# Kernel tuning notes

Measured on AMD Instinct MI355X. Metric: run time of the kernel, lower is better.

Reference implementation:

```python
import jax, jax.numpy as jnp
import numpy as np
import math

B, T, C, H = 4, 2048, 1024, 16

def setup_inputs() -> dict:
    key = jax.random.key(0)
    k1, k2, k3 = jax.random.split(key, 3)
    scale = 1.0 / math.sqrt(C)
    return {
        "x": jax.random.normal(k1, (B, T, C), dtype=jnp.float32),
        "w_attn": jax.random.normal(k2, (C, 3 * C), dtype=jnp.float32) * scale,
        "b_attn": jnp.zeros((3 * C,), dtype=jnp.float32),
        "w_proj": jax.random.normal(k3, (C, C), dtype=jnp.float32) * scale,
        "b_proj": jnp.zeros((C,), dtype=jnp.float32),
    }

def reference(x, w_attn, b_attn, w_proj, b_proj):
    Bq, Tq, Cq = x.shape
    hd = Cq // H  # head dim
    qkv = x @ w_attn + b_attn                       # [B,T,3C]
    q, k, v = jnp.split(qkv, 3, axis=-1)
    # [B,T,C] -> [B,H,T,hd]
    q = q.reshape(Bq, Tq, H, hd).transpose(0, 2, 1, 3)
    k = k.reshape(Bq, Tq, H, hd).transpose(0, 2, 1, 3)
    v = v.reshape(Bq, Tq, H, hd).transpose(0, 2, 1, 3)
    att = jnp.einsum('bhqd,bhkd->bhqk', q, k) * (1.0 / math.sqrt(hd))
    causal = jnp.tril(jnp.ones((Tq, Tq), dtype=bool))
    att = jnp.where(causal[None, None], att, -jnp.inf)
    att = jax.nn.softmax(att, axis=-1)              # dropout p=0 (eval)
    y = jnp.einsum('bhqk,bhkd->bhqd', att, v)       # [B,H,T,hd]
    y = y.transpose(0, 2, 1, 3).reshape(Bq, Tq, Cq)
    return y @ w_proj + b_proj
```

## Files before the change

### kernel.cpp

```cpp
#include <hip/hip_runtime.h>


#define T_SEQ 2048
#define NB 4
#define NH 16
#define CDIM 1024
#define HD 64
#define BH (NB * NH)
#define QSCALE 0.1803368801111204f

typedef float f32x4 __attribute__((ext_vector_type(4)));
typedef float f32x16 __attribute__((ext_vector_type(16)));
typedef __bf16 bf16x8 __attribute__((ext_vector_type(8)));
typedef unsigned short u16x8 __attribute__((ext_vector_type(8)));
typedef unsigned short u16x4 __attribute__((ext_vector_type(4)));

__device__ __forceinline__ unsigned short f2b(float f) {
    union { float f; unsigned u; } v; v.f = f;
    unsigned u = v.u;
    u += 0x7FFFu + ((u >> 16) & 1u);
    return (unsigned short)(u >> 16);
}

__device__ __forceinline__ f32x4 fzero4() {
    f32x4 z; z[0] = 0.f; z[1] = 0.f; z[2] = 0.f; z[3] = 0.f; return z;
}

__device__ __forceinline__ f32x4 mfma16(bf16x8 a, bf16x8 b, f32x4 c) {
    return __builtin_amdgcn_mfma_f32_16x16x32_bf16(a, b, c, 0, 0, 0);
}

__device__ __forceinline__ f32x16 mfma32(bf16x8 a, bf16x8 b, f32x16 c) {
    return __builtin_amdgcn_mfma_f32_32x32x16_bf16(a, b, c, 0, 0, 0);
}

__device__ __forceinline__ void gld16(const void* gp, void* lp) {
    __builtin_amdgcn_global_load_lds(
        (const __attribute__((address_space(1))) unsigned int*)gp,
        (__attribute__((address_space(3))) unsigned int*)lp, 16, 0, 0);
}

#define FENCE asm volatile("" ::: "memory")

__device__ __forceinline__ void transpose_tile(
        const float* __restrict__ in, unsigned short* __restrict__ out,
        int R, int C, int bx, int by) {
    __shared__ unsigned short tile[32][33];
    int tx = threadIdx.x & 31, ty = threadIdx.x >> 5;
    int c0 = bx * 32, r0 = by * 32;
#pragma unroll
    for (int rr = ty; rr < 32; rr += 8)
        tile[rr][tx] = f2b(in[(size_t)(r0 + rr) * C + c0 + tx]);
    __syncthreads();
#pragma unroll
    for (int rr = ty; rr < 32; rr += 8)
        out[(size_t)(c0 + rr) * R + r0 + tx] = tile[tx][rr];
}

__global__ __launch_bounds__(256) void prep_kernel(
        const float* __restrict__ x, const float* __restrict__ wa,
        const float* __restrict__ wp, unsigned short* __restrict__ xb,
        unsigned short* __restrict__ wTa, unsigned short* __restrict__ wTp) {
    int b = blockIdx.x;
    if (b < 1024) {
        int n8 = (NB * T_SEQ * CDIM) / 8;
        for (int i = b * 256 + threadIdx.x; i < n8; i += 1024 * 256) {
            const float4* p = reinterpret_cast<const float4*>(x) + (size_t)i * 2;
            float4 a = p[0], c = p[1];
            u16x8 o;
            o[0] = f2b(a.x); o[1] = f2b(a.y); o[2] = f2b(a.z); o[3] = f2b(a.w);
            o[4] = f2b(c.x); o[5] = f2b(c.y); o[6] = f2b(c.z); o[7] = f2b(c.w);
            *(reinterpret_cast<u16x8*>(xb) + i) = o;
        }
    } else if (b < 1024 + 3072) {
        int t = b - 1024;
        transpose_tile(wa, wTa, 1024, 3072, t % 96, t / 96);
    } else {
        int t = b - 4096;
        transpose_tile(wp, wTp, 1024, 1024, t % 32, t / 32);
    }
}

__global__ __launch_bounds__(256) void gemm_qkv_kernel(
        const unsigned short* __restrict__ A, const unsigned short* __restrict__ Bt,
        const float* __restrict__ bias,
        unsigned short* __restrict__ q_out, unsigned short* __restrict__ k_out,
        unsigned short* __restrict__ v_out, int M, int N, int K) {
    __shared__ alignas(16) unsigned short As[128 * 32];
    __shared__ alignas(16) unsigned short Bs[2][128 * 32];

    int tid = threadIdx.x;
    int wid = tid >> 6, lane = tid & 63;
    int g = lane >> 4, lc = lane & 15;
    int wr = (wid >> 1) * 64, wc = (wid & 1) * 64;
    int m0 = blockIdx.y * 128, n0 = blockIdx.x * 128;

    f32x4 acc[4][4];
#pragma unroll
    for (int m = 0; m < 4; ++m)
#pragma unroll
        for (int n = 0; n < 4; ++n) acc[m][n] = fzero4();

    int srow = tid >> 2;
    int scol = ((tid & 3) ^ ((srow >> 1) & 3)) * 8;
    const unsigned short* Ap = A + (size_t)(m0 + srow) * K + scol;
    const unsigned short* Bp = Bt + (size_t)(n0 + srow) * K + scol;
    int ldst = (wid * 16) * 32;
    int ldst2 = (64 + wid * 16) * 32;

#define STAGE_A(KOFF) {                                    \
        gld16(Ap + (KOFF), &As[ldst]);                     \
        gld16(Ap + (size_t)64 * K + (KOFF), &As[ldst2]); }
#define STAGE_B(BUF, KOFF) {                                       \
        gld16(Bp + (KOFF), &Bs[BUF][ldst]);                        \
        gld16(Bp + (size_t)64 * K + (KOFF), &Bs[BUF][ldst2]); }

    STAGE_B(0, 0)
    STAGE_A(0)
    STAGE_B(1, 32)

    int swz8 = (g ^ ((lc >> 1) & 3)) * 8;

    int nk = K >> 5;
    for (int it = 0; it < nk; ++it) {
        if (it + 1 < nk) { asm volatile("s_waitcnt vmcnt(2)" ::: "memory"); }
        else             { asm volatile("s_waitcnt vmcnt(0)" ::: "memory"); }
        FENCE; __builtin_amdgcn_s_barrier(); FENCE;

        bf16x8 af[4], bfr[4];
        const unsigned short* Bb = Bs[it & 1];
#pragma unroll
        for (int m = 0; m < 4; ++m)
            af[m] = *(const bf16x8*)&As[(wr + m * 16 + lc) * 32 + swz8];
#pragma unroll
        for (int n = 0; n < 4; ++n)
            bfr[n] = *(const bf16x8*)&Bb[(wc + n * 16 + lc) * 32 + swz8];

        __builtin_amdgcn_s_setprio(1);
#pragma unroll
        for (int m = 0; m < 4; ++m)
#pragma unroll
            for (int n = 0; n < 4; ++n)
                acc[m][n] = mfma16(af[m], bfr[n], acc[m][n]);
        __builtin_amdgcn_s_setprio(0);

        asm volatile("s_waitcnt lgkmcnt(0)" ::: "memory");
        FENCE; __builtin_amdgcn_s_barrier(); FENCE;
        if (it + 1 < nk) STAGE_A((it + 1) << 5)
        if (it + 2 < nk) STAGE_B(it & 1, (it + 2) << 5)
    }
#undef STAGE_A
#undef STAGE_B

#pragma unroll
    for (int m = 0; m < 4; ++m) {
        int rowb = m0 + wr + m * 16 + g * 4;
#pragma unroll
        for (int n = 0; n < 4; ++n) {
            int col = n0 + wc + n * 16 + lc;
            float bv = bias[col];
            int which = col >> 10;
            int c = col & 1023;
            int h = c >> 6, d = c & 63;
            int bh_ = (rowb >> 11) * NH + h;
            int tl = rowb & 2047;
            if (which == 2) {
                u16x4 vq;
#pragma unroll
                for (int i = 0; i < 4; ++i) vq[i] = f2b(acc[m][n][i] + bv);
                *(u16x4*)&v_out[(size_t)bh_ * (HD * T_SEQ) + (size_t)d * T_SEQ + tl] = vq;
            } else {
                unsigned short* dst = which ? k_out : q_out;
                float sc = which ? 1.0f : QSCALE;
#pragma unroll
                for (int i = 0; i < 4; ++i)
                    dst[((size_t)bh_ * T_SEQ + tl + i) * HD + d] =
                        f2b((acc[m][n][i] + bv) * sc);
            }
        }
    }
}

__global__ __launch_bounds__(256) void gemm_proj_kernel(
        const unsigned short* __restrict__ A, const unsigned short* __restrict__ Bt,
        const float* __restrict__ bias, float* __restrict__ outF, int M, int N, int K) {
    __shared__ alignas(16) unsigned short As[2][128 * 32];
    __shared__ alignas(16) unsigned short Bs[2][128 * 32];

    int tid = threadIdx.x;
    int wid = tid >> 6, lane = tid & 63;
    int g = lane >> 4, lc = lane & 15;
    int wr = (wid >> 1) * 64, wc = (wid & 1) * 64;
    int m0 = blockIdx.y * 128, n0 = blockIdx.x * 128;

    f32x4 acc[4][4];
#pragma unroll
    for (int m = 0; m < 4; ++m)
#pragma unroll
        for (int n = 0; n < 4; ++n) acc[m][n] = fzero4();

    int srow = tid >> 2;
    int scol = ((tid & 3) ^ ((srow >> 1) & 3)) * 8;
    const unsigned short* Ap = A + (size_t)(m0 + srow) * K + scol;
    const unsigned short* Bp = Bt + (size_t)(n0 + srow) * K + scol;
    int ldst = (wid * 16) * 32;
    int ldst2 = (64 + wid * 16) * 32;

#define GSTAGE(BUF, KOFF)                                      \
    gld16(Ap + (KOFF), &As[BUF][ldst]);                        \
    gld16(Ap + (size_t)64 * K + (KOFF), &As[BUF][ldst2]);      \
    gld16(Bp + (KOFF), &Bs[BUF][ldst]);                        \
    gld16(Bp + (size_t)64 * K + (KOFF), &Bs[BUF][ldst2]);

    GSTAGE(0, 0)
    GSTAGE(1, 32)

    int swz8 = (g ^ ((lc >> 1) & 3)) * 8;

    int nk = K >> 5;
    for (int it = 0; it < nk; ++it) {
        int cur = it & 1;
        if (it + 1 < nk) { asm volatile("s_waitcnt vmcnt(4)" ::: "memory"); }
        else             { asm volatile("s_waitcnt vmcnt(0)" ::: "memory"); }
        FENCE; __builtin_amdgcn_s_barrier(); FENCE;

        bf16x8 af[4], bfr[4];
#pragma unroll
        for (int m = 0; m < 4; ++m)
            af[m] = *(const bf16x8*)&As[cur][(wr + m * 16 + lc) * 32 + swz8];
#pragma unroll
        for (int n = 0; n < 4; ++n)
            bfr[n] = *(const bf16x8*)&Bs[cur][(wc + n * 16 + lc) * 32 + swz8];

        __builtin_amdgcn_s_setprio(1);
#pragma unroll
        for (int m = 0; m < 4; ++m)
#pragma unroll
            for (int n = 0; n < 4; ++n)
                acc[m][n] = mfma16(af[m], bfr[n], acc[m][n]);
        __builtin_amdgcn_s_setprio(0);

        FENCE; __builtin_amdgcn_s_barrier(); FENCE;
        if (it + 2 < nk) { GSTAGE(cur, (it + 2) << 5) }
    }
#undef GSTAGE

#pragma unroll
    for (int m = 0; m < 4; ++m) {
        int rowb = m0 + wr + m * 16 + g * 4;
#pragma unroll
        for (int n = 0; n < 4; ++n) {
            int col = n0 + wc + n * 16 + lc;
            float bv = bias[col];
#pragma unroll
            for (int i = 0; i < 4; ++i)
                outF[(size_t)(rowb + i) * N + col] = acc[m][n][i] + bv;
        }
    }
}

__global__ __launch_bounds__(512, 4) void attn32_kernel(
        const unsigned short* __restrict__ Qb, const unsigned short* __restrict__ Kb,
        const unsigned short* __restrict__ Vt, unsigned short* __restrict__ Yb) {
    __shared__ alignas(16) char smem[32768];

    int tid = threadIdx.x;
    int wid = tid >> 6, lane = tid & 63;
    int ql = lane & 31, hi = lane >> 5;
    int ql7 = ql & 7;

    int id = blockIdx.x;
    int x = id & 7;
    int k = id >> 3;
    int g = k & 7;
    if (k & 32) g = 7 - g;
    int bh = x * 8 + (k >> 3);
    size_t hb = (size_t)bh * (T_SEQ * HD);

    int qt = g * 8 + wid;
    int q0 = qt * 32;
    int ktMax = qt >> 1;
    int ntB = 4 * g + 4;

    bf16x8 qf[4];
    const unsigned short* Qp = Qb + hb + (size_t)(q0 + ql) * HD + hi * 8;
#pragma unroll
    for (int d = 0; d < 4; ++d) qf[d] = *(const bf16x8*)(Qp + d * 16);

    f32x16 zz;
#pragma unroll
    for (int rr = 0; rr < 16; ++rr) zz[rr] = 0.f;
    f32x16 o0 = zz, o1 = zz;
    float mi = -__builtin_inff(), li = 0.f;

    int r8 = lane >> 3;
    int sslot8 = ((lane & 7) ^ r8) * 8;
    const unsigned short* Kg = Kb + hb + (size_t)(wid * 8 + r8) * HD + sslot8;
    const unsigned short* Vg = Vt + hb + (size_t)(wid * 8 + r8) * T_SEQ + sslot8;

    gld16(Kg, smem + wid * 1024);
    gld16(Vg, smem + 8192 + wid * 1024);
    __syncthreads();

#define KF(K0, D) (*(const bf16x8*)&KB_[(((K0)*32 + ql) << 6) + ((((D)*2 + hi) ^ ql7) << 3)])
#define VF(DB, T) (*(const bf16x8*)&VB_[(((DB)*32 + ql) << 6) + ((((T)*2 + hi) ^ ql7) << 3)])

    for (int kt = 0; kt < ntB; ++kt) {
        int cur = kt & 1;
        bool pf = (kt + 1 < ntB);
        if (pf) {
            char* nb = smem + (cur ^ 1) * 16384;
            gld16(Kg + (size_t)(kt + 1) * 64 * HD, nb + wid * 1024);
            gld16(Vg + (kt + 1) * 64, nb + 8192 + wid * 1024);
        }
        if (pf) { asm volatile("s_waitcnt vmcnt(2)" ::: "memory"); }
        else    { asm volatile("s_waitcnt vmcnt(0)" ::: "memory"); }
        FENCE; __builtin_amdgcn_s_barrier(); FENCE;

        if (kt <= ktMax) {
            const unsigned short* KB_ = (const unsigned short*)(smem + cur * 16384);
            const unsigned short* VB_ = (const unsigned short*)(smem + cur * 16384 + 8192);
            int k0 = kt * 64;

            f32x16 s0_, s1_;
            __builtin_amdgcn_s_setprio(1);
            s0_ = mfma32(KF(0, 0), qf[0], zz);
            s0_ = mfma32(KF(0, 1), qf[1], s0_);
            s0_ = mfma32(KF(0, 2), qf[2], s0_);
            s0_ = mfma32(KF(0, 3), qf[3], s0_);
            s1_ = mfma32(KF(1, 0), qf[0], zz);
            s1_ = mfma32(KF(1, 1), qf[1], s1_);
            s1_ = mfma32(KF(1, 2), qf[2], s1_);
            s1_ = mfma32(KF(1, 3), qf[3], s1_);
            __builtin_amdgcn_s_setprio(0);

            if (kt == ktMax) {
                int qg_ = q0 + ql;
#pragma unroll
                for (int rr = 0; rr < 16; ++rr) {
                    int kof_ = k0 + 8 * (rr >> 2) + (rr & 3) + 4 * hi;
                    if (kof_ > qg_) s0_[rr] = -__builtin_inff();
                    if (kof_ + 32 > qg_) s1_[rr] = -__builtin_inff();
                }
            }

            float t_[8];
#pragma unroll
            for (int rr = 0; rr < 8; ++rr)
                t_[rr] = fmaxf(fmaxf(s0_[rr], s0_[rr + 8]), fmaxf(s1_[rr], s1_[rr + 8]));
#pragma unroll
            for (int rr = 0; rr < 4; ++rr) t_[rr] = fmaxf(t_[rr], t_[rr + 4]);
            float pm_ = fmaxf(fmaxf(t_[0], t_[1]), fmaxf(t_[2], t_[3]));
            pm_ = fmaxf(pm_, __shfl_xor(pm_, 32));

            float mn_ = mi;
            if (!__all((int)(pm_ <= mi + 8.f))) {
                mn_ = fmaxf(mi, pm_);
                float f_ = __builtin_amdgcn_exp2f(mi - mn_);
                mi = mn_;
                li *= f_;
                o0 *= f_;
                o1 *= f_;
            }
#pragma unroll
            for (int rr = 0; rr < 16; ++rr) {
                s0_[rr] = __builtin_amdgcn_exp2f(s0_[rr] - mn_);
                s1_[rr] = __builtin_amdgcn_exp2f(s1_[rr] - mn_);
            }
            float u_[8];
#pragma unroll
            for (int rr = 0; rr < 8; ++rr)
                u_[rr] = (s0_[rr] + s0_[rr + 8]) + (s1_[rr] + s1_[rr + 8]);
#pragma unroll
            for (int rr = 0; rr < 4; ++rr) u_[rr] += u_[rr + 4];
            float ps_ = (u_[0] + u_[1]) + (u_[2] + u_[3]);
            ps_ += __shfl_xor(ps_, 32);
            li += ps_;

#pragma unroll
            for (int K0_ = 0; K0_ < 2; ++K0_) {
#pragma unroll
                for (int h2_ = 0; h2_ < 2; ++h2_) {
                    float e0_ = K0_ ? s1_[8 * h2_ + 0] : s0_[8 * h2_ + 0];
                    float e1_ = K0_ ? s1_[8 * h2_ + 1] : s0_[8 * h2_ + 1];
                    float e2_ = K0_ ? s1_[8 * h2_ + 2] : s0_[8 * h2_ + 2];
                    float e3_ = K0_ ? s1_[8 * h2_ + 3] : s0_[8 * h2_ + 3];
                    float e4_ = K0_ ? s1_[8 * h2_ + 4] : s0_[8 * h2_ + 4];
                    float e5_ = K0_ ? s1_[8 * h2_ + 5] : s0_[8 * h2_ + 5];
                    float e6_ = K0_ ? s1_[8 * h2_ + 6] : s0_[8 * h2_ + 6];
                    float e7_ = K0_ ? s1_[8 * h2_ + 7] : s0_[8 * h2_ + 7];
                    unsigned a_, b_, c_, d_;
                    asm("v_cvt_pk_bf16_f32 %0, %1, %2" : "=v"(a_) : "v"(e0_), "v"(e1_));
                    asm("v_cvt_pk_bf16_f32 %0, %1, %2" : "=v"(b_) : "v"(e2_), "v"(e3_));
                    asm("v_cvt_pk_bf16_f32 %0, %1, %2" : "=v"(c_) : "v"(e4_), "v"(e5_));
                    asm("v_cvt_pk_bf16_f32 %0, %1, %2" : "=v"(d_) : "v"(e6_), "v"(e7_));
                    asm("v_permlane32_swap_b32 %0, %1" : "+v"(a_), "+v"(c_));
                    asm("v_permlane32_swap_b32 %0, %1" : "+v"(b_), "+v"(d_));
                    union { unsigned u[4]; bf16x8 v; } pf_;
                    pf_.u[0] = a_; pf_.u[1] = b_; pf_.u[2] = c_; pf_.u[3] = d_;
                    __builtin_amdgcn_s_setprio(1);
                    o0 = mfma32(VF(0, K0_ * 2 + h2_), pf_.v, o0);
                    o1 = mfma32(VF(1, K0_ * 2 + h2_), pf_.v, o1);
                    __builtin_amdgcn_s_setprio(0);
                }
            }
        }
        asm volatile("s_waitcnt lgkmcnt(0)" ::: "memory");
        FENCE; __builtin_amdgcn_s_barrier(); FENCE;
    }
#undef KF
#undef VF

    int bb = bh >> 4, h = bh & 15;
    float iv = 1.0f / li;
#pragma unroll
    for (int dblk = 0; dblk < 2; ++dblk) {
#pragma unroll
        for (int a = 0; a < 4; ++a) {
            u16x4 wv;
#pragma unroll
            for (int i = 0; i < 4; ++i)
                wv[i] = f2b((dblk ? o1[4 * a + i] : o0[4 * a + i]) * iv);
            int dq = dblk * 32 + 8 * a + 4 * hi;
            *(u16x4*)&Yb[((size_t)(bb * T_SEQ + q0 + ql)) * CDIM + h * HD + dq] = wv;
        }
    }
}

extern "C" void kernel_launch(void* const* d_in, const int* in_sizes, int n_in,
                              void* d_out, int out_size, void* d_ws, size_t ws_size,
                              hipStream_t stream) {
    const float* x      = (const float*)d_in[0];
    const float* w_attn = (const float*)d_in[1];
    const float* b_attn = (const float*)d_in[2];
    const float* w_proj = (const float*)d_in[3];
    const float* b_proj = (const float*)d_in[4];
    float* out = (float*)d_out;

    char* ws = (char*)d_ws;
    unsigned short* xb  = (unsigned short*)(ws);
    unsigned short* wTa = (unsigned short*)(ws + 16777216);
    unsigned short* wTp = (unsigned short*)(ws + 23068672);
    unsigned short* qb  = (unsigned short*)(ws + 25165824);
    unsigned short* kb  = (unsigned short*)(ws + 41943040);
    unsigned short* vTb = (unsigned short*)(ws + 58720256);
    unsigned short* yb  = xb;

    prep_kernel<<<dim3(5120), 256, 0, stream>>>(x, w_attn, w_proj, xb, wTa, wTp);

    gemm_qkv_kernel<<<dim3(3072 / 128, 8192 / 128), 256, 0, stream>>>(
        xb, wTa, b_attn, qb, kb, vTb, 8192, 3072, 1024);

    attn32_kernel<<<dim3(512), 512, 0, stream>>>(qb, kb, vTb, yb);

    gemm_proj_kernel<<<dim3(1024 / 128, 8192 / 128), 256, 0, stream>>>(
        yb, wTp, b_proj, out, 8192, 1024, 1024);
}
```

Before: 166.4 us.

## Stage 128-key K/V tiles per barrier in attention kernel

Doubles the per-iteration K/V tile from 64 to 128 keys, so each block runs half as many outer iterations and barriers. Shared memory grows to 64 KB for double-buffered 128-key tiles, with a new V swizzle layout over 128-element rows. The diagonal tile processes one or two 64-key sub-steps depending on the query tile. Larger shared memory use may cut the number of blocks resident per CU, and the coarser granularity adds some wasted loads on diagonal tiles.

```diff
diff --git a/kernel.cpp b/kernel.cpp
--- a/kernel.cpp
+++ b/kernel.cpp
@@ -262,7 +262,7 @@
 __global__ __launch_bounds__(512, 4) void attn32_kernel(
         const unsigned short* __restrict__ Qb, const unsigned short* __restrict__ Kb,
         const unsigned short* __restrict__ Vt, unsigned short* __restrict__ Yb) {
-    __shared__ alignas(16) char smem[32768];
+    __shared__ alignas(16) char smem[65536];
 
     int tid = threadIdx.x;
     int wid = tid >> 6, lane = tid & 63;
@@ -279,8 +279,9 @@
 
     int qt = g * 8 + wid;
     int q0 = qt * 32;
-    int ktMax = qt >> 1;
-    int ntB = 4 * g + 4;
+    int ktMax = qt >> 2;
+    int ntB = 2 * g + 2;
+    int nsubDiag = ((qt & 3) >= 2) ? 2 : 1;
 
     bf16x8 qf[4];
     const unsigned short* Qp = Qb + hb + (size_t)(q0 + ql) * HD + hi * 8;
@@ -293,115 +294,130 @@
     f32x16 o0 = zz, o1 = zz;
     float mi = -__builtin_inff(), li = 0.f;
 
-    int r8 = lane >> 3;
-    int sslot8 = ((lane & 7) ^ r8) * 8;
-    const unsigned short* Kg = Kb + hb + (size_t)(wid * 8 + r8) * HD + sslot8;
-    const unsigned short* Vg = Vt + hb + (size_t)(wid * 8 + r8) * T_SEQ + sslot8;
+    int kr = wid * 8 + (lane >> 3);
+    int kslot8 = ((lane & 7) ^ (kr & 7)) * 8;
+    const unsigned short* Kg = Kb + hb + (size_t)kr * HD + kslot8;
+    int vr = wid * 4 + (lane >> 4);
+    int vslot8 = ((lane & 15) ^ (vr & 7)) * 8;
+    const unsigned short* Vg = Vt + hb + (size_t)vr * T_SEQ + vslot8;
 
     gld16(Kg, smem + wid * 1024);
-    gld16(Vg, smem + 8192 + wid * 1024);
+    gld16(Kg + (size_t)64 * HD, smem + 8192 + wid * 1024);
+    gld16(Vg, smem + 16384 + wid * 1024);
+    gld16(Vg + (size_t)32 * T_SEQ, smem + 16384 + 8192 + wid * 1024);
     __syncthreads();
 
 #define KF(K0, D) (*(const bf16x8*)&KB_[(((K0)*32 + ql) << 6) + ((((D)*2 + hi) ^ ql7) << 3)])
-#define VF(DB, T) (*(const bf16x8*)&VB_[(((DB)*32 + ql) << 6) + ((((T)*2 + hi) ^ ql7) << 3)])
+#define VF(DB, SL) (*(const bf16x8*)&VB_[(((DB)*32 + ql) << 7) + (((SL) ^ ql7) << 3)])
 
     for (int kt = 0; kt < ntB; ++kt) {
         int cur = kt & 1;
         bool pf = (kt + 1 < ntB);
         if (pf) {
-            char* nb = smem + (cur ^ 1) * 16384;
-            gld16(Kg + (size_t)(kt + 1) * 64 * HD, nb + wid * 1024);
-            gld16(Vg + (kt + 1) * 64, nb + 8192 + wid * 1024);
-        }
-        if (pf) { asm volatile("s_waitcnt vmcnt(2)" ::: "memory"); }
+            char* nb = smem + (cur ^ 1) * 32768;
+            int k0n = (kt + 1) << 7;
+            gld16(Kg + (size_t)k0n * HD, nb + wid * 1024);
+            gld16(Kg + (size_t)(k0n + 64) * HD, nb + 8192 + wid * 1024);
+            gld16(Vg + k0n, nb + 16384 + wid * 1024);
+            gld16(Vg + (size_t)32 * T_SEQ + k0n, nb + 16384 + 8192 + wid * 1024);
+        }
+        if (pf) { asm volatile("s_waitcnt vmcnt(4)" ::: "memory"); }
         else    { asm volatile("s_waitcnt vmcnt(0)" ::: "memory"); }
         FENCE; __builtin_amdgcn_s_barrier(); FENCE;
 
         if (kt <= ktMax) {
-            const unsigned short* KB_ = (const unsigned short*)(smem + cur * 16384);
-            const unsigned short* VB_ = (const unsigned short*)(smem + cur * 16384 + 8192);
-            int k0 = kt * 64;
-
-            f32x16 s0_, s1_;
-            __builtin_amdgcn_s_setprio(1);
-            s0_ = mfma32(KF(0, 0), qf[0], zz);
-            s0_ = mfma32(KF(0, 1), qf[1], s0_);
-            s0_ = mfma32(KF(0, 2), qf[2], s0_);
-            s0_ = mfma32(KF(0, 3), qf[3], s0_);
-            s1_ = mfma32(KF(1, 0), qf[0], zz);
-            s1_ = mfma32(KF(1, 1), qf[1], s1_);
-            s1_ = mfma32(KF(1, 2), qf[2], s1_);
-            s1_ = mfma32(KF(1, 3), qf[3], s1_);
-            __builtin_amdgcn_s_setprio(0);
-
-            if (kt == ktMax) {
-                int qg_ = q0 + ql;
+            const unsigned short* KB_ = (const unsigned short*)(smem + cur * 32768);
+            const unsigned short* VB_ = (const unsigned short*)(smem + cur * 32768 + 16384);
+            int k0 = kt << 7;
+            bool diagT = (kt == ktMax);
+            int nsub = diagT ? nsubDiag : 2;
+
+            for (int sub = 0; sub < nsub; ++sub) {
+                int kb_ = k0 + (sub << 6);
+                int K0b = sub * 2;
+
+                f32x16 s0_, s1_;
+                __builtin_amdgcn_s_setprio(1);
+                s0_ = mfma32(KF(K0b, 0), qf[0], zz);
+                s0_ = mfma32(KF(K0b, 1), qf[1], s0_);
+                s0_ = mfma32(KF(K0b, 2), qf[2], s0_);
+                s0_ = mfma32(KF(K0b, 3), qf[3], s0_);
+                s1_ = mfma32(KF(K0b + 1, 0), qf[0], zz);
+                s1_ = mfma32(KF(K0b + 1, 1), qf[1], s1_);
+                s1_ = mfma32(KF(K0b + 1, 2), qf[2], s1_);
+                s1_ = mfma32(KF(K0b + 1, 3), qf[3], s1_);
+                __builtin_amdgcn_s_setprio(0);
+
+                if (diagT && sub == nsub - 1) {
+                    int qg_ = q0 + ql;
+#pragma unroll
+                    for (int rr = 0; rr < 16; ++rr) {
+                        int kof_ = kb_ + 8 * (rr >> 2) + (rr & 3) + 4 * hi;
+                        if (kof_ > qg_) s0_[rr] = -__builtin_inff();
+                        if (kof_ + 32 > qg_) s1_[rr] = -__builtin_inff();
+                    }
+                }
+
+                float t_[8];
+#pragma unroll
+                for (int rr = 0; rr < 8; ++rr)
+                    t_[rr] = fmaxf(fmaxf(s0_[rr], s0_[rr + 8]), fmaxf(s1_[rr], s1_[rr + 8]));
+#pragma unroll
+                for (int rr = 0; rr < 4; ++rr) t_[rr] = fmaxf(t_[rr], t_[rr + 4]);
+                float pm_ = fmaxf(fmaxf(t_[0], t_[1]), fmaxf(t_[2], t_[3]));
+                pm_ = fmaxf(pm_, __shfl_xor(pm_, 32));
+
+                float mn_ = mi;
+                if (!__all((int)(pm_ <= mi + 8.f))) {
+                    mn_ = fmaxf(mi, pm_);
+                    float f_ = __builtin_amdgcn_exp2f(mi - mn_);
+                    mi = mn_;
+                    li *= f_;
+                    o0 *= f_;
+                    o1 *= f_;
+                }
 #pragma unroll
                 for (int rr = 0; rr < 16; ++rr) {
-                    int kof_ = k0 + 8 * (rr >> 2) + (rr & 3) + 4 * hi;
-                    if (kof_ > qg_) s0_[rr] = -__builtin_inff();
-                    if (kof_ + 32 > qg_) s1_[rr] = -__builtin_inff();
+                    s0_[rr] = __builtin_amdgcn_exp2f(s0_[rr] - mn_);
+                    s1_[rr] = __builtin_amdgcn_exp2f(s1_[rr] - mn_);
                 }
-            }
-
-            float t_[8];
-#pragma unroll
-            for (int rr = 0; rr < 8; ++rr)
-                t_[rr] = fmaxf(fmaxf(s0_[rr], s0_[rr + 8]), fmaxf(s1_[rr], s1_[rr + 8]));
-#pragma unroll
-            for (int rr = 0; rr < 4; ++rr) t_[rr] = fmaxf(t_[rr], t_[rr + 4]);
-            float pm_ = fmaxf(fmaxf(t_[0], t_[1]), fmaxf(t_[2], t_[3]));
-            pm_ = fmaxf(pm_, __shfl_xor(pm_, 32));
-
-            float mn_ = mi;
-            if (!__all((int)(pm_ <= mi + 8.f))) {
-                mn_ = fmaxf(mi, pm_);
-                float f_ = __builtin_amdgcn_exp2f(mi - mn_);
-                mi = mn_;
-                li *= f_;
-                o0 *= f_;
-                o1 *= f_;
-            }
-#pragma unroll
-            for (int rr = 0; rr < 16; ++rr) {
-                s0_[rr] = __builtin_amdgcn_exp2f(s0_[rr] - mn_);
-                s1_[rr] = __builtin_amdgcn_exp2f(s1_[rr] - mn_);
-            }
-            float u_[8];
-#pragma unroll
-            for (int rr = 0; rr < 8; ++rr)
-                u_[rr] = (s0_[rr] + s0_[rr + 8]) + (s1_[rr] + s1_[rr + 8]);
-#pragma unroll
-            for (int rr = 0; rr < 4; ++rr) u_[rr] += u_[rr + 4];
-            float ps_ = (u_[0] + u_[1]) + (u_[2] + u_[3]);
-            ps_ += __shfl_xor(ps_, 32);
-            li += ps_;
-
-#pragma unroll
-            for (int K0_ = 0; K0_ < 2; ++K0_) {
-#pragma unroll
-                for (int h2_ = 0; h2_ < 2; ++h2_) {
-                    float e0_ = K0_ ? s1_[8 * h2_ + 0] : s0_[8 * h2_ + 0];
-                    float e1_ = K0_ ? s1_[8 * h2_ + 1] : s0_[8 * h2_ + 1];
-                    float e2_ = K0_ ? s1_[8 * h2_ + 2] : s0_[8 * h2_ + 2];
-                    float e3_ = K0_ ? s1_[8 * h2_ + 3] : s0_[8 * h2_ + 3];
-                    float e4_ = K0_ ? s1_[8 * h2_ + 4] : s0_[8 * h2_ + 4];
-                    float e5_ = K0_ ? s1_[8 * h2_ + 5] : s0_[8 * h2_ + 5];
-                    float e6_ = K0_ ? s1_[8 * h2_ + 6] : s0_[8 * h2_ + 6];
-                    float e7_ = K0_ ? s1_[8 * h2_ + 7] : s0_[8 * h2_ + 7];
-                    unsigned a_, b_, c_, d_;
-                    asm("v_cvt_pk_bf16_f32 %0, %1, %2" : "=v"(a_) : "v"(e0_), "v"(e1_));
-                    asm("v_cvt_pk_bf16_f32 %0, %1, %2" : "=v"(b_) : "v"(e2_), "v"(e3_));
-                    asm("v_cvt_pk_bf16_f32 %0, %1, %2" : "=v"(c_) : "v"(e4_), "v"(e5_));
-                    asm("v_cvt_pk_bf16_f32 %0, %1, %2" : "=v"(d_) : "v"(e6_), "v"(e7_));
-                    asm("v_permlane32_swap_b32 %0, %1" : "+v"(a_), "+v"(c_));
-                    asm("v_permlane32_swap_b32 %0, %1" : "+v"(b_), "+v"(d_));
-                    union { unsigned u[4]; bf16x8 v; } pf_;
-                    pf_.u[0] = a_; pf_.u[1] = b_; pf_.u[2] = c_; pf_.u[3] = d_;
-                    __builtin_amdgcn_s_setprio(1);
-                    o0 = mfma32(VF(0, K0_ * 2 + h2_), pf_.v, o0);
-                    o1 = mfma32(VF(1, K0_ * 2 + h2_), pf_.v, o1);
-                    __builtin_amdgcn_s_setprio(0);
+                float u_[8];
+#pragma unroll
+                for (int rr = 0; rr < 8; ++rr)
+                    u_[rr] = (s0_[rr] + s0_[rr + 8]) + (s1_[rr] + s1_[rr + 8]);
+#pragma unroll
+                for (int rr = 0; rr < 4; ++rr) u_[rr] += u_[rr + 4];
+                float ps_ = (u_[0] + u_[1]) + (u_[2] + u_[3]);
+                ps_ += __shfl_xor(ps_, 32);
+                li += ps_;
+
+#pragma unroll
+                for (int K0_ = 0; K0_ < 2; ++K0_) {
+#pragma unroll
+                    for (int h2_ = 0; h2_ < 2; ++h2_) {
+                        float e0_ = K0_ ? s1_[8 * h2_ + 0] : s0_[8 * h2_ + 0];
+                        float e1_ = K0_ ? s1_[8 * h2_ + 1] : s0_[8 * h2_ + 1];
+                        float e2_ = K0_ ? s1_[8 * h2_ + 2] : s0_[8 * h2_ + 2];
+                        float e3_ = K0_ ? s1_[8 * h2_ + 3] : s0_[8 * h2_ + 3];
+                        float e4_ = K0_ ? s1_[8 * h2_ + 4] : s0_[8 * h2_ + 4];
+                        float e5_ = K0_ ? s1_[8 * h2_ + 5] : s0_[8 * h2_ + 5];
+                        float e6_ = K0_ ? s1_[8 * h2_ + 6] : s0_[8 * h2_ + 6];
+                        float e7_ = K0_ ? s1_[8 * h2_ + 7] : s0_[8 * h2_ + 7];
+                        unsigned a_, b_, c_, d_;
+                        asm("v_cvt_pk_bf16_f32 %0, %1, %2" : "=v"(a_) : "v"(e0_), "v"(e1_));
+                        asm("v_cvt_pk_bf16_f32 %0, %1, %2" : "=v"(b_) : "v"(e2_), "v"(e3_));
+                        asm("v_cvt_pk_bf16_f32 %0, %1, %2" : "=v"(c_) : "v"(e4_), "v"(e5_));
+                        asm("v_cvt_pk_bf16_f32 %0, %1, %2" : "=v"(d_) : "v"(e6_), "v"(e7_));
+                        asm("v_permlane32_swap_b32 %0, %1" : "+v"(a_), "+v"(c_));
+                        asm("v_permlane32_swap_b32 %0, %1" : "+v"(b_), "+v"(d_));
+                        union { unsigned u[4]; bf16x8 v; } pf_;
+                        pf_.u[0] = a_; pf_.u[1] = b_; pf_.u[2] = c_; pf_.u[3] = d_;
+                        int sl_ = (sub << 3) + (K0_ * 2 + h2_) * 2 + hi;
+                        __builtin_amdgcn_s_setprio(1);
+                        o0 = mfma32(VF(0, sl_), pf_.v, o0);
+                        o1 = mfma32(VF(1, sl_), pf_.v, o1);
+                        __builtin_amdgcn_s_setprio(0);
+                    }
                 }
             }
         }
```

Result: no change. 169.3 us (+1.7%).
